# Kernel tuning notes

Hardware: AMD Instinct MI355X
Metric: run time of the kernel (lower is better)

Reference implementation:

```python
import jax, jax.numpy as jnp
import numpy as np

B, T, N, F = 4, 24, 1024, 128
EPS = 1e-5  # torch nn.LayerNorm default
FRONT_T = 12  # hard-coded graph_array[:12] split in the original module
MIN_NUMBER = 3  # hard-coded topk k


def setup_inputs() -> dict:
    key = jax.random.key(0)
    ks = jax.random.split(key, 7)
    sc = 0.05
    return {
        "input": jax.random.normal(ks[0], (B, T, N, F), jnp.float32),
        # torch nn.Linear stores weight as [out, in]; y = x @ W.T + b
        "W_xff": jax.random.normal(ks[1], (3 * F, F), jnp.float32) * sc,
        "b_xff": jax.random.normal(ks[2], (3 * F,), jnp.float32) * sc,
        "W_ff1": jax.random.normal(ks[3], (F, F), jnp.float32) * sc,
        "b_ff1": jnp.zeros((F,), jnp.float32),
        "W_ff2": jax.random.normal(ks[4], (F, F), jnp.float32) * sc,
        "b_ff2": jnp.zeros((F,), jnp.float32),
        "ln_g": jnp.ones((F,), jnp.float32),
        "ln_b": jnp.zeros((F,), jnp.float32),
    }


def _mixup_last(front, y):
    # front: [12, N, F]; y: scalar int (data-dependent column index).
    # mixup_region with block_size=1: replace column y with the mean of
    # columns [max(y-1,0), min(y+2,N)), cast through uint8 (as original).
    n = front.shape[1]
    y_start = jnp.maximum(y - 1, 0)
    y_end = jnp.minimum(y + 2, n)
    cols = jnp.arange(n)
    mask = ((cols >= y_start) & (cols < y_end)).astype(front.dtype)  # [N]
    cnt = (y_end - y_start).astype(front.dtype)
    mixed = (front * mask[None, :, None]).sum(axis=1) / cnt  # [12, F]
    # .to(torch.uint8) truncates and kills gradient for this column
    mixed = jax.lax.stop_gradient(mixed.astype(jnp.uint8).astype(front.dtype))
    return front.at[:, y, :].set(mixed)


def reference(input, W_xff, b_xff, W_ff1, b_ff1, W_ff2, b_ff2, ln_g, ln_b):
    f = input.shape[-1]
    x_ = input @ W_xff.T + b_xff  # [B,T,N,3F]
    q, k, v = x_[..., :f], x_[..., f:2 * f], x_[..., 2 * f:]
    e = jnp.einsum('btnf,btmf->btnm', q, k) / jnp.sqrt(jnp.asarray(f, x_.dtype))
    attn = jax.nn.softmax(e, axis=-1)  # [B,T,N,N]

    # detached attention maps drive the topk row selection
    attn_d = jax.lax.stop_gradient(attn)
    col_sums = attn_d.sum(axis=2)  # torch sum(dim=1) per [T,N,N] -> [B,T,N]
    # torch.topk(largest=False, sorted=True): 3 smallest, ascending by value
    _, idx = jax.lax.top_k(-col_sums, MIN_NUMBER)  # [B,T,3]
    # NOTE: the original loop reassigns `graph_array = mixup_region(graph_array_front, ...)`
    # each iteration, so only the LAST mixup (i = T-1, 3rd smallest index) survives.
    y_last = idx[:, -1, -1]  # [B]

    front = v[:, :FRONT_T]   # [B,12,N,F]
    back = v[:, FRONT_T:]    # [B,T-12,N,F]
    new_front = jax.vmap(_mixup_last)(front, y_last)
    new_value = jnp.concatenate([new_front, back], axis=1)  # [B,T,N,F]

    value_i = jnp.einsum('btnm,btmf->btnf', attn, new_value)
    h = jax.nn.gelu(value_i @ W_ff1.T + b_ff1, approximate=False) @ W_ff2.T + b_ff2
    res = h + input
    mu = res.mean(-1, keepdims=True)
    var = ((res - mu) ** 2).mean(-1, keepdims=True)
    return (res - mu) / jnp.sqrt(var + EPS) * ln_g + ln_b
```

## Files before the change

### kernel.cpp

```cpp
#include <hip/hip_runtime.h>
#include <math.h>

#define BB 4
#define TT 24
#define BN 1024
#define FD 128
#define BT (BB*TT)
#define BTN (BT*BN)
#define FRONT_T 12
#define SCALE 0.08838834764831845f
#define GELU_K 0.7071067811865476f

typedef __attribute__((ext_vector_type(8))) short s8v;
typedef __attribute__((ext_vector_type(4))) float f4v;

static __device__ __forceinline__ unsigned short f2bf(float f) {
    union { float f; unsigned u; } c; c.f = f;
    unsigned u = c.u + 0x7FFFu + ((c.u >> 16) & 1u);
    return (unsigned short)(u >> 16);
}

__global__ __launch_bounds__(256) void k_convx(const float* __restrict__ x,
                                               unsigned short* __restrict__ xb) {
    size_t i = ((size_t)blockIdx.x * 256 + threadIdx.x) * 4;
    float4 v = *(const float4*)(x + i);
    ushort4 h = {f2bf(v.x), f2bf(v.y), f2bf(v.z), f2bf(v.w)};
    *(ushort4*)(xb + i) = h;
}

__global__ void k_convw(const float* __restrict__ W, unsigned short* __restrict__ wb, int n) {
    int i = blockIdx.x * 256 + threadIdx.x;
    if (i < n) wb[i] = f2bf(W[i]);
}

__global__ __launch_bounds__(256, 2) void k_qkv_mfma(
    const unsigned short* __restrict__ xb, const unsigned short* __restrict__ wb,
    const float* __restrict__ bias,
    unsigned short* __restrict__ qb16, unsigned short* __restrict__ kb16,
    unsigned short* __restrict__ vtb)
{
    __shared__ __attribute__((aligned(16))) unsigned short Xs[64 * 136];
    __shared__ __attribute__((aligned(16))) unsigned short Ws[64 * 136];
    __shared__ __attribute__((aligned(16))) unsigned short Cs[64 * 72];
    const int tid = threadIdx.x;
    const int rowBase = blockIdx.x * 64;
    const int colBase = blockIdx.y * 64;
    const int lane = tid & 63, wave = tid >> 6;
    const int lx = lane & 15, quad = lane >> 4;

    for (int i = 0; i < 4; ++i) {
        int idx = i * 256 + tid, r = idx >> 4, c8 = idx & 15;
        *(int4*)(&Xs[r * 136 + c8 * 8]) = *(const int4*)(xb + (size_t)(rowBase + r) * FD + c8 * 8);
    }
    for (int i = 0; i < 4; ++i) {
        int idx = i * 256 + tid, r = idx >> 4, c8 = idx & 15;
        *(int4*)(&Ws[r * 136 + c8 * 8]) = *(const int4*)(wb + (size_t)(colBase + r) * FD + c8 * 8);
    }
    __syncthreads();

    f4v acc[4];
    for (int gg = 0; gg < 4; ++gg) acc[gg] = (f4v){0.f, 0.f, 0.f, 0.f};
    for (int t4 = 0; t4 < 4; ++t4) {
        s8v a = *(const s8v*)(&Xs[(wave * 16 + lx) * 136 + t4 * 32 + quad * 8]);
        for (int gg = 0; gg < 4; ++gg) {
            s8v b = *(const s8v*)(&Ws[(gg * 16 + lx) * 136 + t4 * 32 + quad * 8]);
            acc[gg] = __builtin_amdgcn_mfma_f32_16x16x32_bf16(a, b, acc[gg], 0, 0, 0);
        }
    }

    const int n0 = wave * 16 + quad * 4;
    if (colBase < 2 * FD) {
        for (int gg = 0; gg < 4; ++gg) {
            float bb = bias[colBase + gg * 16 + lx];
            for (int r = 0; r < 4; ++r)
                Cs[(n0 + r) * 72 + gg * 16 + lx] = f2bf(acc[gg][r] + bb);
        }
        __syncthreads();
        unsigned short* dst = (colBase < FD) ? qb16 : kb16;
        const int cc0 = colBase & (FD - 1);
        for (int i = 0; i < 2; ++i) {
            int idx = i * 256 + tid, r = idx >> 3, c8 = idx & 7;
            *(int4*)(dst + (size_t)(rowBase + r) * FD + cc0 + c8 * 8) =
                *(const int4*)(&Cs[r * 72 + c8 * 8]);
        }
    } else {
        for (int gg = 0; gg < 4; ++gg) {
            float bb = bias[colBase + gg * 16 + lx];
            for (int r = 0; r < 4; ++r)
                Cs[(gg * 16 + lx) * 72 + n0 + r] = f2bf(acc[gg][r] + bb);
        }
        __syncthreads();
        const int bt = rowBase >> 10, nBase = rowBase & 1023, cc0 = colBase - 2 * FD;
        for (int i = 0; i < 2; ++i) {
            int idx = i * 256 + tid, f = idx >> 3, c8 = idx & 7;
            *(int4*)(vtb + ((size_t)bt * FD + cc0 + f) * BN + nBase + c8 * 8) =
                *(const int4*)(&Cs[f * 72 + c8 * 8]);
        }
    }
}

__global__ __launch_bounds__(256) void k_qkv32(const float* __restrict__ x,
                                               const float* __restrict__ W,
                                               const float* __restrict__ bias,
                                               float* __restrict__ q32c,
                                               float* __restrict__ k32c) {
    __shared__ float Xs[32][129];
    __shared__ float Ws[64][129];
    const int tid = threadIdx.x;
    const int b = blockIdx.x >> 5;
    const int rt = blockIdx.x & 31;
    const int xrow0 = (b * TT + (TT - 1)) * BN + rt * 32;
    const int colBase = blockIdx.y * 64;

    for (int i = 0; i < 4; ++i) {
        int idx = i * 256 + tid;
        int r = idx >> 5, c4 = idx & 31;
        *(float4*)(&Xs[r][c4 * 4]) = *(const float4*)(x + (size_t)(xrow0 + r) * FD + c4 * 4);
    }
    for (int i = 0; i < 8; ++i) {
        int idx = i * 256 + tid;
        int r = idx >> 5, c4 = idx & 31;
        *(float4*)(&Ws[r][c4 * 4]) = *(const float4*)(W + (size_t)(colBase + r) * FD + c4 * 4);
    }
    __syncthreads();

    const int tx = tid & 15, ty = tid >> 4;
    const int r0 = ty * 2, r1 = ty * 2 + 1;
    float acc0[4] = {0.f, 0.f, 0.f, 0.f};
    float acc1[4] = {0.f, 0.f, 0.f, 0.f};
    for (int kk = 0; kk < FD; ++kk) {
        float a0 = Xs[r0][kk], a1 = Xs[r1][kk];
        float b0 = Ws[tx * 4 + 0][kk];
        float b1 = Ws[tx * 4 + 1][kk];
        float b2 = Ws[tx * 4 + 2][kk];
        float b3 = Ws[tx * 4 + 3][kk];
        acc0[0] += a0 * b0; acc0[1] += a0 * b1; acc0[2] += a0 * b2; acc0[3] += a0 * b3;
        acc1[0] += a1 * b0; acc1[1] += a1 * b1; acc1[2] += a1 * b2; acc1[3] += a1 * b3;
    }
    const int c = colBase + tx * 4;
    float4 bia = *(const float4*)(bias + c);
    float* dst = (c < FD) ? q32c : k32c;
    int cc = (c < FD) ? c : c - FD;
    size_t base = ((size_t)b * BN + rt * 32 + r0) * FD + cc;
    *(float4*)(dst + base)      = make_float4(acc0[0] + bia.x, acc0[1] + bia.y, acc0[2] + bia.z, acc0[3] + bia.w);
    *(float4*)(dst + base + FD) = make_float4(acc1[0] + bia.x, acc1[1] + bia.y, acc1[2] + bia.z, acc1[3] + bia.w);
}

__global__ __launch_bounds__(256) void k_pass1(const float* __restrict__ q32c,
                                               const float* __restrict__ k32c,
                                               float* __restrict__ Mp,
                                               float* __restrict__ Lp) {
    __shared__ float Qs[32][129];
    __shared__ float Ks[64][129];
    const int tid = threadIdx.x;
    const int chunk = blockIdx.y;
    const int b = blockIdx.z;
    const int rowBase = blockIdx.x * 32;
    const float* qb = q32c + (size_t)b * BN * FD;
    const float* kb = k32c + (size_t)b * BN * FD;

    for (int i = 0; i < 4; ++i) {
        int idx = i * 256 + tid;
        int r = idx >> 5, c4 = idx & 31;
        *(float4*)(&Qs[r][c4 * 4]) = *(const float4*)(qb + (size_t)(rowBase + r) * FD + c4 * 4);
    }
    const int tx = tid & 15, ty = tid >> 4;
    const int r0 = ty * 2, r1 = ty * 2 + 1;
    float m[2] = {-1e30f, -1e30f};
    float l[2] = {0.f, 0.f};

    for (int ct = chunk * 4; ct < chunk * 4 + 4; ++ct) {
        __syncthreads();
        for (int i = 0; i < 8; ++i) {
            int idx = i * 256 + tid;
            int r = idx >> 5, c4 = idx & 31;
            *(float4*)(&Ks[r][c4 * 4]) = *(const float4*)(kb + (size_t)(ct * 64 + r) * FD + c4 * 4);
        }
        __syncthreads();
        float e0[4] = {0.f, 0.f, 0.f, 0.f};
        float e1[4] = {0.f, 0.f, 0.f, 0.f};
        for (int kk = 0; kk < FD; ++kk) {
            float a0 = Qs[r0][kk], a1 = Qs[r1][kk];
            float b0 = Ks[tx * 4 + 0][kk];
            float b1 = Ks[tx * 4 + 1][kk];
            float b2 = Ks[tx * 4 + 2][kk];
            float b3 = Ks[tx * 4 + 3][kk];
            e0[0] += a0 * b0; e0[1] += a0 * b1; e0[2] += a0 * b2; e0[3] += a0 * b3;
            e1[0] += a1 * b0; e1[1] += a1 * b1; e1[2] += a1 * b2; e1[3] += a1 * b3;
        }
        float* ep[2] = {e0, e1};
        for (int rr = 0; rr < 2; ++rr) {
            float s0 = ep[rr][0] * SCALE, s1 = ep[rr][1] * SCALE;
            float s2 = ep[rr][2] * SCALE, s3 = ep[rr][3] * SCALE;
            float tm = fmaxf(fmaxf(s0, s1), fmaxf(s2, s3));
            for (int s = 1; s < 16; s <<= 1) tm = fmaxf(tm, __shfl_xor(tm, s, 64));
            float ts = __expf(s0 - tm) + __expf(s1 - tm) + __expf(s2 - tm) + __expf(s3 - tm);
            for (int s = 1; s < 16; s <<= 1) ts += __shfl_xor(ts, s, 64);
            float mn = fmaxf(m[rr], tm);
            l[rr] = l[rr] * __expf(m[rr] - mn) + ts * __expf(tm - mn);
            m[rr] = mn;
        }
    }
    if (tx == 0) {
        size_t base = (size_t)chunk * BB * BN + (size_t)b * BN + rowBase;
        Mp[base + r0] = m[0];
        Lp[base + r0] = l[0];
        Mp[base + r1] = m[1];
        Lp[base + r1] = l[1];
    }
}

__global__ void k_mergeML(const float* __restrict__ Mp, const float* __restrict__ Lp,
                          float* __restrict__ Mv, float* __restrict__ Lv) {
    int i = blockIdx.x * 256 + threadIdx.x;
    if (i >= BB * BN) return;
    float m = -1e30f, l = 0.f;
    for (int c = 0; c < 4; ++c) {
        float mc = Mp[(size_t)c * BB * BN + i];
        float lc = Lp[(size_t)c * BB * BN + i];
        float mn = fmaxf(m, mc);
        l = l * __expf(m - mn) + lc * __expf(mc - mn);
        m = mn;
    }
    Mv[i] = m;
    Lv[i] = l;
}

__global__ __launch_bounds__(256) void k_colsum(const float* __restrict__ q32c,
                                                const float* __restrict__ k32c,
                                                const float* __restrict__ Mv,
                                                const float* __restrict__ Lv,
                                                float* __restrict__ csp) {
    __shared__ float Qs[32][129];
    __shared__ float Ks[64][129];
    __shared__ float red[16][68];
    const int tid = threadIdx.x;
    const int rchunk = blockIdx.y;
    const int b = blockIdx.z;
    const int colBase = blockIdx.x * 64;
    const float* qb = q32c + (size_t)b * BN * FD;
    const float* kb = k32c + (size_t)b * BN * FD;
    const int tx = tid & 15, ty = tid >> 4;
    const int r0 = ty * 2, r1 = ty * 2 + 1;

    for (int i = 0; i < 8; ++i) {
        int idx = i * 256 + tid;
        int r = idx >> 5, c4 = idx & 31;
        *(float4*)(&Ks[r][c4 * 4]) = *(const float4*)(kb + (size_t)(colBase + r) * FD + c4 * 4);
    }

    float acc[4] = {0.f, 0.f, 0.f, 0.f};
    for (int rt = rchunk * 4; rt < rchunk * 4 + 4; ++rt) {
        __syncthreads();
        for (int i = 0; i < 4; ++i) {
            int idx = i * 256 + tid;
            int r = idx >> 5, c4 = idx & 31;
            *(float4*)(&Qs[r][c4 * 4]) = *(const float4*)(qb + (size_t)(rt * 32 + r) * FD + c4 * 4);
        }
        __syncthreads();
        float e0[4] = {0.f, 0.f, 0.f, 0.f};
        float e1[4] = {0.f, 0.f, 0.f, 0.f};
        for (int kk = 0; kk < FD; ++kk) {
            float a0 = Qs[r0][kk], a1 = Qs[r1][kk];
            float b0 = Ks[tx * 4 + 0][kk];
            float b1 = Ks[tx * 4 + 1][kk];
            float b2 = Ks[tx * 4 + 2][kk];
            float b3 = Ks[tx * 4 + 3][kk];
            e0[0] += a0 * b0; e0[1] += a0 * b1; e0[2] += a0 * b2; e0[3] += a0 * b3;
            e1[0] += a1 * b0; e1[1] += a1 * b1; e1[2] += a1 * b2; e1[3] += a1 * b3;
        }
        int n0 = rt * 32 + r0, n1 = rt * 32 + r1;
        float m0 = Mv[(size_t)b * BN + n0], il0 = 1.0f / Lv[(size_t)b * BN + n0];
        float m1 = Mv[(size_t)b * BN + n1], il1 = 1.0f / Lv[(size_t)b * BN + n1];
        for (int j = 0; j < 4; ++j) {
            acc[j] += __expf(e0[j] * SCALE - m0) * il0;
            acc[j] += __expf(e1[j] * SCALE - m1) * il1;
        }
    }
    for (int j = 0; j < 4; ++j) red[ty][tx * 4 + j] = acc[j];
    __syncthreads();
    if (tid < 64) {
        float s = 0.f;
        for (int i = 0; i < 16; ++i) s += red[i][tid];
        csp[((size_t)rchunk * BB + b) * BN + colBase + tid] = s;
    }
}

__global__ void k_top3(const float* __restrict__ csp, int* __restrict__ ylast) {
    __shared__ float sv[192];
    __shared__ int si[192];
    const int b = blockIdx.x;
    const int t = threadIdx.x;
    float bv[3] = {1e30f, 1e30f, 1e30f};
    int bi[3] = {0x7fffffff, 0x7fffffff, 0x7fffffff};
    for (int i = 0; i < 16; ++i) {
        int idx = t * 16 + i;
        float vv = 0.f;
        for (int c = 0; c < 8; ++c)
            vv += csp[((size_t)c * BB + b) * BN + idx];
        if (vv < bv[0]) {
            bv[2] = bv[1]; bi[2] = bi[1];
            bv[1] = bv[0]; bi[1] = bi[0];
            bv[0] = vv;    bi[0] = idx;
        } else if (vv < bv[1]) {
            bv[2] = bv[1]; bi[2] = bi[1];
            bv[1] = vv;    bi[1] = idx;
        } else if (vv < bv[2]) {
            bv[2] = vv;    bi[2] = idx;
        }
    }
    for (int j = 0; j < 3; ++j) { sv[t * 3 + j] = bv[j]; si[t * 3 + j] = bi[j]; }
    __syncthreads();
    if (t == 0) {
        float fv[3] = {1e30f, 1e30f, 1e30f};
        int fi[3] = {0x7fffffff, 0x7fffffff, 0x7fffffff};
        for (int c = 0; c < 192; ++c) {
            float vv = sv[c]; int ii = si[c];
            if (vv < fv[0] || (vv == fv[0] && ii < fi[0])) {
                fv[2] = fv[1]; fi[2] = fi[1];
                fv[1] = fv[0]; fi[1] = fi[0];
                fv[0] = vv;    fi[0] = ii;
            } else if (vv < fv[1] || (vv == fv[1] && ii < fi[1])) {
                fv[2] = fv[1]; fi[2] = fi[1];
                fv[1] = vv;    fi[1] = ii;
            } else if (vv < fv[2] || (vv == fv[2] && ii < fi[2])) {
                fv[2] = vv;    fi[2] = ii;
            }
        }
        ylast[b] = fi[2];
    }
}

__global__ void k_mixup(const float* __restrict__ x, const float* __restrict__ W,
                        const float* __restrict__ bias,
                        unsigned short* __restrict__ vtb,
                        const int* __restrict__ ylast) {
    const int b = blockIdx.y, t = blockIdx.x, f = threadIdx.x;
    const int y = ylast[b];
    const int ys = max(y - 1, 0), ye = min(y + 2, BN);
    const float* wrow = W + (size_t)(2 * FD + f) * FD;
    const float bia = bias[2 * FD + f];
    float s = 0.f;
    for (int r = ys; r < ye; ++r) {
        const float* xrow = x + ((size_t)(b * TT + t) * BN + r) * FD;
        float acc = 0.f;
        for (int kk = 0; kk < FD; ++kk) acc += xrow[kk] * wrow[kk];
        s += acc + bia;
    }
    s /= (float)(ye - ys);
    int ti = (int)s;
    unsigned u = ((unsigned)ti) & 0xFFu;
    vtb[((size_t)(b * TT + t) * FD + f) * BN + y] = f2bf((float)u);
}

__global__ __launch_bounds__(256, 3) void k_flash(
    const unsigned short* __restrict__ qb, const unsigned short* __restrict__ kb,
    const unsigned short* __restrict__ vtb, float* __restrict__ vi)
{
    __shared__ __attribute__((aligned(16))) unsigned short Ks[64 * 136];
    __shared__ __attribute__((aligned(16))) unsigned short Vts[128 * 72];
    __shared__ __attribute__((aligned(16))) unsigned short Ps[4][16 * 72];
    const int tid = threadIdx.x;
    const int f = blockIdx.y * 8 + blockIdx.x;
    const int s = (f & 7) * 96 + (f >> 3);
    const int bt = s >> 3;
    const int rowBase = (s & 7) * 128;
    const int lane = tid & 63, wave = tid >> 6;
    const int lx = lane & 15, quad = lane >> 4;

    const unsigned short* qg = qb + ((size_t)bt * BN + rowBase) * FD;
    s8v aq[2][4];
    #pragma unroll
    for (int rg = 0; rg < 2; ++rg)
        #pragma unroll
        for (int t4 = 0; t4 < 4; ++t4)
            aq[rg][t4] = *(const s8v*)(qg + (size_t)(rg * 64 + wave * 16 + lx) * FD + t4 * 32 + quad * 8);

    f4v O[2][8];
    #pragma unroll
    for (int rg = 0; rg < 2; ++rg)
        for (int gg = 0; gg < 8; ++gg) O[rg][gg] = (f4v){0.f, 0.f, 0.f, 0.f};
    float mrow[2][4] = {{-1e30f, -1e30f, -1e30f, -1e30f}, {-1e30f, -1e30f, -1e30f, -1e30f}};
    float lrow[2][4] = {{0.f, 0.f, 0.f, 0.f}, {0.f, 0.f, 0.f, 0.f}};

    const unsigned short* kgbase = kb + (size_t)bt * BN * FD;
    const unsigned short* vgbase = vtb + (size_t)bt * FD * BN;

    for (int ct = 0; ct < 16; ++ct) {
        __syncthreads();
        const unsigned short* kg = kgbase + (size_t)ct * 64 * FD;
        for (int i = 0; i < 4; ++i) {
            int idx = i * 256 + tid, r = idx >> 4, c8 = idx & 15;
            *(int4*)(&Ks[r * 136 + c8 * 8]) = *(const int4*)(kg + r * FD + c8 * 8);
        }
        for (int i = 0; i < 4; ++i) {
            int idx = i * 256 + tid, r = idx >> 3, c8 = idx & 7;
            *(int4*)(&Vts[r * 72 + c8 * 8]) = *(const int4*)(vgbase + (size_t)r * BN + ct * 64 + c8 * 8);
        }
        __syncthreads();

        #pragma unroll
        for (int rg = 0; rg < 2; ++rg) {
            f4v e[4];
            for (int n4 = 0; n4 < 4; ++n4) {
                f4v acc = (f4v){0.f, 0.f, 0.f, 0.f};
                for (int t4 = 0; t4 < 4; ++t4) {
                    s8v bk = *(const s8v*)(&Ks[(n4 * 16 + lx) * 136 + t4 * 32 + quad * 8]);
                    acc = __builtin_amdgcn_mfma_f32_16x16x32_bf16(aq[rg][t4], bk, acc, 0, 0, 0);
                }
                for (int r = 0; r < 4; ++r) acc[r] *= SCALE;
                e[n4] = acc;
            }
            for (int r = 0; r < 4; ++r) {
                float tm = fmaxf(fmaxf(e[0][r], e[1][r]), fmaxf(e[2][r], e[3][r]));
                for (int s2 = 1; s2 < 16; s2 <<= 1) tm = fmaxf(tm, __shfl_xor(tm, s2, 64));
                float mn = fmaxf(mrow[rg][r], tm);
                float alpha = __expf(mrow[rg][r] - mn);
                mrow[rg][r] = mn;
                float ps = 0.f;
                for (int n4 = 0; n4 < 4; ++n4) {
                    float p = __expf(e[n4][r] - mn);
                    e[n4][r] = p;
                    ps += p;
                }
                for (int s2 = 1; s2 < 16; s2 <<= 1) ps += __shfl_xor(ps, s2, 64);
                lrow[rg][r] = lrow[rg][r] * alpha + ps;
                for (int gg = 0; gg < 8; ++gg) O[rg][gg][r] *= alpha;
            }
            for (int n4 = 0; n4 < 4; ++n4)
                for (int r = 0; r < 4; ++r)
                    Ps[wave][(quad * 4 + r) * 72 + n4 * 16 + lx] = f2bf(e[n4][r]);
            for (int k2 = 0; k2 < 2; ++k2) {
                s8v ap = *(const s8v*)(&Ps[wave][lx * 72 + k2 * 32 + quad * 8]);
                for (int gg = 0; gg < 8; ++gg) {
                    s8v bv = *(const s8v*)(&Vts[(gg * 16 + lx) * 72 + k2 * 32 + quad * 8]);
                    O[rg][gg] = __builtin_amdgcn_mfma_f32_16x16x32_bf16(ap, bv, O[rg][gg], 0, 0, 0);
                }
            }
        }
    }
    #pragma unroll
    for (int rg = 0; rg < 2; ++rg) {
        const int row0 = rowBase + rg * 64 + wave * 16 + quad * 4;
        for (int r = 0; r < 4; ++r) {
            float inv = 1.0f / lrow[rg][r];
            for (int gg = 0; gg < 8; ++gg)
                vi[((size_t)bt * BN + row0 + r) * FD + gg * 16 + lx] = O[rg][gg][r] * inv;
        }
    }
}

__global__ __launch_bounds__(256) void k_ffn(const float* __restrict__ vi,
                                             const float* __restrict__ x,
                                             const float* __restrict__ W1,
                                             const float* __restrict__ b1,
                                             const float* __restrict__ W2,
                                             const float* __restrict__ b2,
                                             const float* __restrict__ g,
                                             const float* __restrict__ lb,
                                             float* __restrict__ out) {
    __shared__ float Qs[32][132];
    __shared__ float KVs[64][132];
    const int tid = threadIdx.x;
    const int bt = blockIdx.y;
    const int rowBase = blockIdx.x * 32;
    const int tx = tid & 15, ty = tid >> 4;
    const int r0 = ty * 2, r1 = ty * 2 + 1;

    const float* vb = vi + ((size_t)bt * BN + rowBase) * FD;
    for (int i = 0; i < 4; ++i) {
        int idx = i * 256 + tid;
        int r = idx >> 5, c4 = idx & 31;
        *(float4*)(&Qs[r][c4 * 4]) = *(const float4*)(vb + (size_t)r * FD + c4 * 4);
    }

    float h0[8], h1[8];
    {
        float t0[8] = {}, t1[8] = {};
        for (int ch = 0; ch < 2; ++ch) {
            __syncthreads();
            for (int i = 0; i < 8; ++i) {
                int idx = i * 256 + tid;
                int r = idx >> 5, c4 = idx & 31;
                *(float4*)(&KVs[r][c4 * 4]) = *(const float4*)(W1 + (size_t)(ch * 64 + r) * FD + c4 * 4);
            }
            __syncthreads();
            for (int kk = 0; kk < FD; ++kk) {
                float u0 = Qs[r0][kk], u1 = Qs[r1][kk];
                for (int jj = 0; jj < 4; ++jj) {
                    int j = jj + 4 * ch;
                    float w = KVs[tx + 16 * jj][kk];
                    t0[j] += u0 * w;
                    t1[j] += u1 * w;
                }
            }
        }
        for (int j = 0; j < 8; ++j) {
            int f = tx + 16 * j;
            float bj = b1[f];
            float z0 = t0[j] + bj, z1 = t1[j] + bj;
            h0[j] = 0.5f * z0 * (1.0f + erff(z0 * GELU_K));
            h1[j] = 0.5f * z1 * (1.0f + erff(z1 * GELU_K));
        }
    }
    __syncthreads();
    for (int j = 0; j < 8; ++j) { Qs[r0][tx + 16 * j] = h0[j]; Qs[r1][tx + 16 * j] = h1[j]; }
    __syncthreads();

    float z0[8], z1[8];
    {
        float t0[8] = {}, t1[8] = {};
        for (int ch = 0; ch < 2; ++ch) {
            __syncthreads();
            for (int i = 0; i < 8; ++i) {
                int idx = i * 256 + tid;
                int r = idx >> 5, c4 = idx & 31;
                *(float4*)(&KVs[r][c4 * 4]) = *(const float4*)(W2 + (size_t)(ch * 64 + r) * FD + c4 * 4);
            }
            __syncthreads();
            for (int kk = 0; kk < FD; ++kk) {
                float u0 = Qs[r0][kk], u1 = Qs[r1][kk];
                for (int jj = 0; jj < 4; ++jj) {
                    int j = jj + 4 * ch;
                    float w = KVs[tx + 16 * jj][kk];
                    t0[j] += u0 * w;
                    t1[j] += u1 * w;
                }
            }
        }
        for (int j = 0; j < 8; ++j) {
            int f = tx + 16 * j;
            float bj = b2[f];
            z0[j] = t0[j] + bj;
            z1[j] = t1[j] + bj;
        }
    }

    const float* xb = x + ((size_t)bt * BN + rowBase) * FD;
    float res0[8], res1[8];
    float s0 = 0.f, s1 = 0.f;
    for (int j = 0; j < 8; ++j) {
        int f = tx + 16 * j;
        res0[j] = z0[j] + xb[(size_t)r0 * FD + f];
        res1[j] = z1[j] + xb[(size_t)r1 * FD + f];
        s0 += res0[j];
        s1 += res1[j];
    }
    for (int s = 1; s < 16; s <<= 1) { s0 += __shfl_xor(s0, s, 64); s1 += __shfl_xor(s1, s, 64); }
    const float mu0 = s0 * (1.0f / FD), mu1 = s1 * (1.0f / FD);
    float q0 = 0.f, q1 = 0.f;
    for (int j = 0; j < 8; ++j) {
        float d0 = res0[j] - mu0, d1 = res1[j] - mu1;
        q0 += d0 * d0;
        q1 += d1 * d1;
    }
    for (int s = 1; s < 16; s <<= 1) { q0 += __shfl_xor(q0, s, 64); q1 += __shfl_xor(q1, s, 64); }
    const float rs0 = rsqrtf(q0 * (1.0f / FD) + 1e-5f);
    const float rs1 = rsqrtf(q1 * (1.0f / FD) + 1e-5f);
    float* ob = out + ((size_t)bt * BN + rowBase) * FD;
    for (int j = 0; j < 8; ++j) {
        int f = tx + 16 * j;
        float gf = g[f], bf = lb[f];
        ob[(size_t)r0 * FD + f] = (res0[j] - mu0) * rs0 * gf + bf;
        ob[(size_t)r1 * FD + f] = (res1[j] - mu1) * rs1 * gf + bf;
    }
}

extern "C" void kernel_launch(void* const* d_in, const int* in_sizes, int n_in,
                              void* d_out, int out_size, void* d_ws, size_t ws_size,
                              hipStream_t stream) {
    const float* x     = (const float*)d_in[0];
    const float* W_xff = (const float*)d_in[1];
    const float* b_xff = (const float*)d_in[2];
    const float* W_ff1 = (const float*)d_in[3];
    const float* b_ff1 = (const float*)d_in[4];
    const float* W_ff2 = (const float*)d_in[5];
    const float* b_ff2 = (const float*)d_in[6];
    const float* ln_g  = (const float*)d_in[7];
    const float* ln_b  = (const float*)d_in[8];
    float* out = (float*)d_out;

    char* w = (char*)d_ws;
    unsigned short* qb16 = (unsigned short*)w;  w += (size_t)BTN * FD * 2;
    unsigned short* kb16 = (unsigned short*)w;  w += (size_t)BTN * FD * 2;
    unsigned short* vtb  = (unsigned short*)w;  w += (size_t)BTN * FD * 2;
    unsigned short* wxb  = (unsigned short*)w;  w += (size_t)3 * FD * FD * 2;
    char* alias = w;
    float* vi = (float*)alias;
    unsigned short* xb = (unsigned short*)alias; alias += (size_t)BTN * FD * 2;
    float* q32c = (float*)alias;                alias += (size_t)BB * BN * FD * 4;
    float* k32c = (float*)alias;                alias += (size_t)BB * BN * FD * 4;
    float* Mv   = (float*)alias;                alias += (size_t)BB * BN * 4;
    float* Lv   = (float*)alias;                alias += (size_t)BB * BN * 4;
    int* ylast  = (int*)alias;                  alias += 256;
    float* Mp   = (float*)alias;                alias += (size_t)4 * BB * BN * 4;
    float* Lp   = (float*)alias;                alias += (size_t)4 * BB * BN * 4;
    float* csp  = (float*)alias;                alias += (size_t)8 * BB * BN * 4;

    k_convx    <<<dim3(BTN * FD / 1024), 256, 0, stream>>>(x, xb);
    k_convw    <<<dim3(192),             256, 0, stream>>>(W_xff, wxb, 3 * FD * FD);
    k_qkv_mfma <<<dim3(BTN / 64, 6),     256, 0, stream>>>(xb, wxb, b_xff, qb16, kb16, vtb);
    k_qkv32    <<<dim3(BB * 32, 4),      256, 0, stream>>>(x, W_xff, b_xff, q32c, k32c);
    k_pass1    <<<dim3(32, 4, BB),       256, 0, stream>>>(q32c, k32c, Mp, Lp);
    k_mergeML  <<<dim3((BB * BN + 255) / 256), 256, 0, stream>>>(Mp, Lp, Mv, Lv);
    k_colsum   <<<dim3(16, 8, BB),       256, 0, stream>>>(q32c, k32c, Mv, Lv, csp);
    k_top3     <<<dim3(BB),               64, 0, stream>>>(csp, ylast);
    k_mixup    <<<dim3(FRONT_T, BB),     128, 0, stream>>>(x, W_xff, b_xff, vtb, ylast);
    k_flash    <<<dim3(8, BT),           256, 0, stream>>>(qb16, kb16, vtb, vi);
    k_ffn      <<<dim3(32, BT),          256, 0, stream>>>(vi, x, W_ff1, b_ff1, W_ff2, b_ff2,
                                                           ln_g, ln_b, out);
}
```

Baseline: 531.9 us.

## Transpose MFMA operands in flash kernel, prefetch K/V tiles into registers

The flash-attention kernel swaps the MFMA operand order so each lane holds one query row. Row max and sum then need only two cross-lane shuffles instead of four per row, and the running max and sum shrink to one scalar per row group. Next K/V tiles are prefetched into registers while the current tile is computed, overlapping global loads with compute. P is written to a swizzled, unpadded LDS buffer with packed 64-bit stores, rescaling is skipped when the max does not change, and the output is written with float4 stores. The cost is more registers held for the prefetch and a data-dependent branch, which could lower occupancy under the 3-blocks launch bound.

```diff
diff --git a/kernel.cpp b/kernel.cpp
--- a/kernel.cpp
+++ b/kernel.cpp
@@ -359,7 +359,7 @@
 {
     __shared__ __attribute__((aligned(16))) unsigned short Ks[64 * 136];
     __shared__ __attribute__((aligned(16))) unsigned short Vts[128 * 72];
-    __shared__ __attribute__((aligned(16))) unsigned short Ps[4][16 * 72];
+    __shared__ __attribute__((aligned(16))) unsigned short Ps[4][16 * 64];
     const int tid = threadIdx.x;
     const int f = blockIdx.y * 8 + blockIdx.x;
     const int s = (f & 7) * 96 + (f >> 3);
@@ -367,6 +367,7 @@
     const int rowBase = (s & 7) * 128;
     const int lane = tid & 63, wave = tid >> 6;
     const int lx = lane & 15, quad = lane >> 4;
+    const int swz = (lx & 7) << 3;
 
     const unsigned short* qg = qb + ((size_t)bt * BN + rowBase) * FD;
     s8v aq[2][4];
@@ -380,72 +381,127 @@
     #pragma unroll
     for (int rg = 0; rg < 2; ++rg)
         for (int gg = 0; gg < 8; ++gg) O[rg][gg] = (f4v){0.f, 0.f, 0.f, 0.f};
-    float mrow[2][4] = {{-1e30f, -1e30f, -1e30f, -1e30f}, {-1e30f, -1e30f, -1e30f, -1e30f}};
-    float lrow[2][4] = {{0.f, 0.f, 0.f, 0.f}, {0.f, 0.f, 0.f, 0.f}};
+    float mrow[2] = {-1e30f, -1e30f};
+    float lrow[2] = {0.f, 0.f};
 
     const unsigned short* kgbase = kb + (size_t)bt * BN * FD;
     const unsigned short* vgbase = vtb + (size_t)bt * FD * BN;
 
+    int4 kreg[4], vreg[4];
+    #pragma unroll
+    for (int i = 0; i < 4; ++i) {
+        int idx = i * 256 + tid, r = idx >> 4, c8 = idx & 15;
+        kreg[i] = *(const int4*)(kgbase + (size_t)r * FD + c8 * 8);
+    }
+    #pragma unroll
+    for (int i = 0; i < 4; ++i) {
+        int idx = i * 256 + tid, r = idx >> 3, c8 = idx & 7;
+        vreg[i] = *(const int4*)(vgbase + (size_t)r * BN + c8 * 8);
+    }
+
     for (int ct = 0; ct < 16; ++ct) {
         __syncthreads();
-        const unsigned short* kg = kgbase + (size_t)ct * 64 * FD;
+        #pragma unroll
         for (int i = 0; i < 4; ++i) {
             int idx = i * 256 + tid, r = idx >> 4, c8 = idx & 15;
-            *(int4*)(&Ks[r * 136 + c8 * 8]) = *(const int4*)(kg + r * FD + c8 * 8);
-        }
+            *(int4*)(&Ks[r * 136 + c8 * 8]) = kreg[i];
+        }
+        #pragma unroll
         for (int i = 0; i < 4; ++i) {
             int idx = i * 256 + tid, r = idx >> 3, c8 = idx & 7;
-            *(int4*)(&Vts[r * 72 + c8 * 8]) = *(const int4*)(vgbase + (size_t)r * BN + ct * 64 + c8 * 8);
+            *(int4*)(&Vts[r * 72 + c8 * 8]) = vreg[i];
+        }
+        if (ct < 15) {
+            const unsigned short* kg = kgbase + (size_t)(ct + 1) * 64 * FD;
+            #pragma unroll
+            for (int i = 0; i < 4; ++i) {
+                int idx = i * 256 + tid, r = idx >> 4, c8 = idx & 15;
+                kreg[i] = *(const int4*)(kg + (size_t)r * FD + c8 * 8);
+            }
+            #pragma unroll
+            for (int i = 0; i < 4; ++i) {
+                int idx = i * 256 + tid, r = idx >> 3, c8 = idx & 7;
+                vreg[i] = *(const int4*)(vgbase + (size_t)r * BN + (ct + 1) * 64 + c8 * 8);
+            }
         }
         __syncthreads();
 
         #pragma unroll
         for (int rg = 0; rg < 2; ++rg) {
             f4v e[4];
+            #pragma unroll
             for (int n4 = 0; n4 < 4; ++n4) {
                 f4v acc = (f4v){0.f, 0.f, 0.f, 0.f};
+                #pragma unroll
                 for (int t4 = 0; t4 < 4; ++t4) {
                     s8v bk = *(const s8v*)(&Ks[(n4 * 16 + lx) * 136 + t4 * 32 + quad * 8]);
-                    acc = __builtin_amdgcn_mfma_f32_16x16x32_bf16(aq[rg][t4], bk, acc, 0, 0, 0);
+                    acc = __builtin_amdgcn_mfma_f32_16x16x32_bf16(bk, aq[rg][t4], acc, 0, 0, 0);
                 }
+                #pragma unroll
                 for (int r = 0; r < 4; ++r) acc[r] *= SCALE;
                 e[n4] = acc;
             }
-            for (int r = 0; r < 4; ++r) {
-                float tm = fmaxf(fmaxf(e[0][r], e[1][r]), fmaxf(e[2][r], e[3][r]));
-                for (int s2 = 1; s2 < 16; s2 <<= 1) tm = fmaxf(tm, __shfl_xor(tm, s2, 64));
-                float mn = fmaxf(mrow[rg][r], tm);
-                float alpha = __expf(mrow[rg][r] - mn);
-                mrow[rg][r] = mn;
-                float ps = 0.f;
-                for (int n4 = 0; n4 < 4; ++n4) {
-                    float p = __expf(e[n4][r] - mn);
-                    e[n4][r] = p;
-                    ps += p;
-                }
-                for (int s2 = 1; s2 < 16; s2 <<= 1) ps += __shfl_xor(ps, s2, 64);
-                lrow[rg][r] = lrow[rg][r] * alpha + ps;
-                for (int gg = 0; gg < 8; ++gg) O[rg][gg][r] *= alpha;
-            }
-            for (int n4 = 0; n4 < 4; ++n4)
-                for (int r = 0; r < 4; ++r)
-                    Ps[wave][(quad * 4 + r) * 72 + n4 * 16 + lx] = f2bf(e[n4][r]);
+            float t0 = fmaxf(fmaxf(e[0][0], e[0][1]), fmaxf(e[0][2], e[0][3]));
+            float t1 = fmaxf(fmaxf(e[1][0], e[1][1]), fmaxf(e[1][2], e[1][3]));
+            float t2 = fmaxf(fmaxf(e[2][0], e[2][1]), fmaxf(e[2][2], e[2][3]));
+            float t3 = fmaxf(fmaxf(e[3][0], e[3][1]), fmaxf(e[3][2], e[3][3]));
+            float tm = fmaxf(fmaxf(t0, t1), fmaxf(t2, t3));
+            tm = fmaxf(tm, __shfl_xor(tm, 16, 64));
+            tm = fmaxf(tm, __shfl_xor(tm, 32, 64));
+            float mo = mrow[rg];
+            float mn = fmaxf(mo, tm);
+            mrow[rg] = mn;
+            float ps0 = 0.f, ps1 = 0.f, ps2 = 0.f, ps3 = 0.f;
+            #pragma unroll
+            for (int n4 = 0; n4 < 4; ++n4) {
+                float p0 = __expf(e[n4][0] - mn);
+                float p1 = __expf(e[n4][1] - mn);
+                float p2 = __expf(e[n4][2] - mn);
+                float p3 = __expf(e[n4][3] - mn);
+                e[n4][0] = p0; e[n4][1] = p1; e[n4][2] = p2; e[n4][3] = p3;
+                ps0 += p0; ps1 += p1; ps2 += p2; ps3 += p3;
+            }
+            float ps = (ps0 + ps1) + (ps2 + ps3);
+            ps += __shfl_xor(ps, 16, 64);
+            ps += __shfl_xor(ps, 32, 64);
+            if (tm > mo) {
+                float alpha = __expf(mo - mn);
+                lrow[rg] = lrow[rg] * alpha + ps;
+                #pragma unroll
+                for (int gg = 0; gg < 8; ++gg)
+                    for (int r = 0; r < 4; ++r) O[rg][gg][r] *= alpha;
+            } else {
+                lrow[rg] += ps;
+            }
+            #pragma unroll
+            for (int n4 = 0; n4 < 4; ++n4) {
+                unsigned w0 = (unsigned)f2bf(e[n4][0]) | ((unsigned)f2bf(e[n4][1]) << 16);
+                unsigned w1 = (unsigned)f2bf(e[n4][2]) | ((unsigned)f2bf(e[n4][3]) << 16);
+                int col = (n4 * 16 + quad * 4) ^ swz;
+                uint2 w = {w0, w1};
+                *(uint2*)(&Ps[wave][lx * 64 + col]) = w;
+            }
+            #pragma unroll
             for (int k2 = 0; k2 < 2; ++k2) {
-                s8v ap = *(const s8v*)(&Ps[wave][lx * 72 + k2 * 32 + quad * 8]);
+                s8v bp = *(const s8v*)(&Ps[wave][lx * 64 + ((k2 * 32 + quad * 8) ^ swz)]);
+                #pragma unroll
                 for (int gg = 0; gg < 8; ++gg) {
                     s8v bv = *(const s8v*)(&Vts[(gg * 16 + lx) * 72 + k2 * 32 + quad * 8]);
-                    O[rg][gg] = __builtin_amdgcn_mfma_f32_16x16x32_bf16(ap, bv, O[rg][gg], 0, 0, 0);
+                    O[rg][gg] = __builtin_amdgcn_mfma_f32_16x16x32_bf16(bv, bp, O[rg][gg], 0, 0, 0);
                 }
             }
         }
     }
     #pragma unroll
     for (int rg = 0; rg < 2; ++rg) {
-        const int row0 = rowBase + rg * 64 + wave * 16 + quad * 4;
-        for (int r = 0; r < 4; ++r) {
-            float inv = 1.0f / lrow[rg][r];
-            for (int gg = 0; gg < 8; ++gg)
-                vi[((size_t)bt * BN + row0 + r) * FD + gg * 16 + lx] = O[rg][gg][r] * inv;
+        const int qglob = rowBase + rg * 64 + wave * 16 + lx;
+        float inv = 1.0f / lrow[rg];
+        float* vrow = vi + ((size_t)bt * BN + qglob) * FD;
+        #pragma unroll
+        for (int gg = 0; gg < 8; ++gg) {
+            float4 o4 = make_float4(O[rg][gg][0] * inv, O[rg][gg][1] * inv,
+                                    O[rg][gg][2] * inv, O[rg][gg][3] * inv);
+            *(float4*)(vrow + gg * 16 + quad * 4) = o4;
         }
     }
 }
```

New measurement: 550.0 us. 3.4% more time.
